# Kernel optimization log

Hardware: AMD Instinct MI355X
Metric: run time of the kernel (lower is better)

## Reference

```python
import jax, jax.numpy as jnp
import numpy as np

NEG_SLOPE = 0.2    # DenseGATConv attention leaky_relu slope (PyG default)
ACT_SLOPE = 0.01   # block activation LeakyReLU slope
HEADS = 3


def setup_inputs() -> dict:
    key = jax.random.key(0)
    B, N, D0, D1, D2, H = 512, 128, 128, 64, 64, HEADS
    ks = jax.random.split(key, 7)
    x = jax.random.normal(ks[0], (B * N, D0), jnp.float32)
    # equal-sized graphs: sorted graph ids, N atoms per graph
    batch_mask = jnp.repeat(jnp.arange(B, dtype=jnp.int32), N)
    s0 = 1.0 / np.sqrt(D0)
    s1 = 1.0 / np.sqrt(D1)
    s2 = 1.0 / np.sqrt(D2)
    W1 = jax.random.normal(ks[1], (D0, H * D1), jnp.float32) * s0
    att_src1 = jax.random.normal(ks[2], (H, D1), jnp.float32) * s1
    att_dst1 = jax.random.normal(ks[3], (H, D1), jnp.float32) * s1
    b1 = jnp.zeros((D1,), jnp.float32)
    W2 = jax.random.normal(ks[4], (D1, H * D2), jnp.float32) * s1
    att_src2 = jax.random.normal(ks[5], (H, D2), jnp.float32) * s2
    att_dst2 = jax.random.normal(ks[6], (H, D2), jnp.float32) * s2
    b2 = jnp.zeros((D2,), jnp.float32)
    return dict(x=x, batch_mask=batch_mask, W1=W1, att_src1=att_src1,
                att_dst1=att_dst1, b1=b1, W2=W2, att_src2=att_src2,
                att_dst2=att_dst2, b2=b2, batch_size=B, n_max=N)


def _dense_gat(x, adj, W, a_src, a_dst, b):
    # x: [B, N, Din], adj: [B, N, N] (self-loops already set). concat=False.
    B, N, _ = x.shape
    H, C = a_src.shape
    h = (x @ W).reshape(B, N, H, C)                       # lin (no bias)
    a_s = jnp.einsum('bnhc,hc->bnh', h, a_src)            # per-node src score
    a_d = jnp.einsum('bnhc,hc->bnh', h, a_dst)            # per-node dst score
    alpha = a_s[:, None, :, :] + a_d[:, :, None, :]       # [B, i, j, H]
    alpha = jax.nn.leaky_relu(alpha, NEG_SLOPE)
    alpha = jnp.where(adj[..., None] == 0, -jnp.inf, alpha)
    alpha = jax.nn.softmax(alpha, axis=2)                 # over source j
    out = jnp.einsum('bijh,bjhc->bihc', alpha, h)         # [B, N, H, C]
    return out.mean(axis=2) + b                           # concat=False -> head mean


def reference(x, batch_mask, W1, att_src1, att_dst1, b1,
              W2, att_src2, att_dst2, b2, batch_size, n_max):
    total, D0 = x.shape
    counts = jnp.bincount(batch_mask, length=batch_size)          # atoms per graph
    starts = jnp.cumsum(counts) - counts
    pos = jnp.arange(total) - starts[batch_mask]                  # slot within graph
    # to_dense_batch
    xd = jnp.zeros((batch_size, n_max, D0), x.dtype).at[batch_mask, pos].set(x)
    node_in = jnp.arange(n_max)[None, :] < counts[:, None]        # [B, N] valid mask
    # block adjacency: fully connected within each graph, diag zeroed...
    adj = (node_in[:, :, None] & node_in[:, None, :]).astype(x.dtype)
    # ...then DenseGATConv add_loop=True re-sets the full diagonal to 1
    adj = jnp.where(jnp.eye(n_max, dtype=bool), jnp.asarray(1.0, x.dtype), adj)
    h = _dense_gat(xd, adj, W1, att_src1, att_dst1, b1)
    h = jax.nn.leaky_relu(h, ACT_SLOPE)
    h = _dense_gat(h, adj, W2, att_src2, att_dst2, b2)
    h = jax.nn.leaky_relu(h, ACT_SLOPE)
    return jnp.sum(h, axis=1)                                     # sum pooling -> [B, D2]
```

## Files before the change

kernel.cpp:

```cpp
#include <hip/hip_runtime.h>
#include <stdint.h>

#define NROW 128

typedef __attribute__((ext_vector_type(8))) __bf16 bf16x8;
typedef __attribute__((ext_vector_type(4))) float  f32x4;

static __device__ __forceinline__ uint16_t f2bf(float f) {
    union { float f; uint32_t i; } v; v.f = f;
    uint32_t x = v.i;
    return (uint16_t)((x + 0x7FFFu + ((x >> 16) & 1u)) >> 16);
}
static __device__ __forceinline__ uint16_t bfbits(float f) {
    __bf16 h = (__bf16)f;
    union { __bf16 h; uint16_t u; } c; c.h = h; return c.u;
}
static __device__ __forceinline__ float fexp2(float x) {
#if __has_builtin(__builtin_amdgcn_exp2f)
    return __builtin_amdgcn_exp2f(x);
#else
    return exp2f(x);
#endif
}
static __device__ __forceinline__ float frcp(float x) {
#if __has_builtin(__builtin_amdgcn_rcpf)
    return __builtin_amdgcn_rcpf(x);
#else
    return 1.0f / x;
#endif
}

__global__ __launch_bounds__(256)
void prep_kernel(const float* __restrict__ W1, const float* __restrict__ as1,
                 const float* __restrict__ ad1,
                 const float* __restrict__ W2, const float* __restrict__ as2,
                 const float* __restrict__ ad2,
                 uint16_t* __restrict__ wT1x, uint16_t* __restrict__ wT2x)
{
    constexpr float LOG2E = 1.4426950408889634f;
    int bid = blockIdx.x, t = threadIdx.x;
    if (bid < 96) {
        int idx = bid * 256 + t;
        int c = idx >> 7, k = idx & 127;
        wT1x[c * 128 + k] = f2bf(W1[k * 192 + c]);
    } else if (bid < 144) {
        int idx = (bid - 96) * 256 + t;
        int c = idx >> 6, k = idx & 63;
        wT2x[c * 64 + k] = f2bf(W2[k * 192 + c]);
    } else if (bid == 144) {
#pragma unroll
        for (int e = 0; e < 3; ++e) {
            int idx = t + e * 256;
            if (idx < 768) {
                int j = idx >> 7, k = idx & 127, hd = j >> 1;
                const float* av = (j & 1) ? ad1 : as1;
                float s = 0.f;
                for (int c = 0; c < 64; ++c)
                    s += W1[k * 192 + hd * 64 + c] * av[hd * 64 + c];
                wT1x[(192 + j) * 128 + k] = f2bf(s * LOG2E);
            }
        }
#pragma unroll
        for (int e = 0; e < 5; ++e) {
            int idx = t + e * 256;
            if (idx < 1280) wT1x[198 * 128 + idx] = 0;
        }
    } else {
#pragma unroll
        for (int e = 0; e < 2; ++e) {
            int idx = t + e * 256;
            if (idx < 384) {
                int j = idx >> 6, k = idx & 63, hd = j >> 1;
                const float* av = (j & 1) ? ad2 : as2;
                float s = 0.f;
                for (int c = 0; c < 64; ++c)
                    s += W2[k * 192 + hd * 64 + c] * av[hd * 64 + c];
                wT2x[(192 + j) * 64 + k] = f2bf(s * LOG2E);
            }
        }
#pragma unroll
        for (int e = 0; e < 3; ++e) {
            int idx = t + e * 256;
            if (idx < 640) wT2x[198 * 64 + idx] = 0;
        }
    }
}

static __device__ __forceinline__ uint32_t hT_off(int row, int colbytes) {
    uint32_t bo = (uint32_t)(row * 256 + colbytes);
    return bo ^ (uint32_t)((row & 7) << 4);
}
#define S2 72

static __device__ __forceinline__
void scores_and_hT(const f32x4* hacc, uint16_t* hT, float* as_s, float* ad_s,
                   int i0, int lr, int lg)
{
    if (lr < 6) {
        float* dst = (lr & 1) ? ad_s : as_s;
        int hd = lr >> 1;
#pragma unroll
        for (int r = 0; r < 4; ++r)
            dst[hd * 128 + i0 + lg * 4 + r] = hacc[12][r];
    }
#pragma unroll
    for (int f = 0; f < 12; ++f) {
        uint32_t p0 = (uint32_t)bfbits(hacc[f][0]) | ((uint32_t)bfbits(hacc[f][1]) << 16);
        uint32_t p1 = (uint32_t)bfbits(hacc[f][2]) | ((uint32_t)bfbits(hacc[f][3]) << 16);
        *(uint2*)((char*)hT + hT_off(f * 16 + lr, (i0 + lg * 4) * 2)) = make_uint2(p0, p1);
    }
}

static __device__ __forceinline__
void softmax_pv(const uint16_t* hT, const float* as_s, const float* ad_s,
                f32x4* oacc, int i0, int lr, int lg)
{
#pragma unroll
    for (int f = 0; f < 4; ++f) oacc[f] = (f32x4){0.f, 0.f, 0.f, 0.f};

#pragma unroll
    for (int hd = 0; hd < 3; ++hd) {
        float ad  = ad_s[hd * 128 + i0 + lr];
        float adm = ad - 16.0f;
        float adn = 0.2f * ad - 16.0f;
        bf16x8 ap[4];
        float zp = 0.f;
#pragma unroll
        for (int q = 0; q < 4; ++q) {
            float4 s0 = *(const float4*)&as_s[hd * 128 + q * 32 + lg * 8];
            float4 s1 = *(const float4*)&as_s[hd * 128 + q * 32 + lg * 8 + 4];
            float sv[8] = {s0.x, s0.y, s0.z, s0.w, s1.x, s1.y, s1.z, s1.w};
#pragma unroll
            for (int m = 0; m < 8; ++m) {
                float ev = fexp2(fmaxf(sv[m] + adm, __builtin_fmaf(sv[m], 0.2f, adn)));
                zp += ev;
                ap[q][m] = (__bf16)ev;
            }
        }
        zp += __shfl_xor(zp, 16);
        zp += __shfl_xor(zp, 32);
        float inv = frcp(3.0f * zp);

        f32x4 tacc[4];
#pragma unroll
        for (int f = 0; f < 4; ++f) tacc[f] = (f32x4){0.f, 0.f, 0.f, 0.f};
#pragma unroll
        for (int q = 0; q < 4; ++q)
#pragma unroll
            for (int f = 0; f < 4; ++f) {
                bf16x8 bfv = *(const bf16x8*)((const char*)hT +
                                 hT_off(hd * 64 + f * 16 + lr, q * 64 + lg * 16));
                tacc[f] = __builtin_amdgcn_mfma_f32_16x16x32_bf16(ap[q], bfv, tacc[f], 0, 0, 0);
            }
        float invr[4];
#pragma unroll
        for (int r = 0; r < 4; ++r) invr[r] = __shfl(inv, lg * 4 + r);
#pragma unroll
        for (int f = 0; f < 4; ++f)
#pragma unroll
            for (int r = 0; r < 4; ++r) oacc[f][r] += tacc[f][r] * invr[r];
    }
}

__global__ __launch_bounds__(512, 4)
void fused_kernel(const float* __restrict__ x,
                  const uint16_t* __restrict__ wT1g, const uint16_t* __restrict__ wT2g,
                  const float* __restrict__ b1g, const float* __restrict__ b2g,
                  float* __restrict__ outp)
{
    __shared__ __align__(16) char smem[49152];
    __shared__ __align__(16) float as_s[3 * 128];
    __shared__ __align__(16) float ad_s[3 * 128];
    __shared__ float bia[128];
    __shared__ float pool_s[8 * 64];

    uint16_t* hT  = (uint16_t*)smem;
    uint16_t* x2T = (uint16_t*)smem;

    const int b = blockIdx.x, t = threadIdx.x;
    const int w = t >> 6, lr = t & 15, lg = (t >> 4) & 3;
    const int i0 = w * 16;

    bf16x8 afr[4];
    {
        const float* xg = x + ((long)b * NROW + i0 + lr) * 128;
        float4 r0[4], r1[4];
#pragma unroll
        for (int q = 0; q < 4; ++q) {
            r0[q] = *(const float4*)(xg + q * 32 + lg * 8);
            r1[q] = *(const float4*)(xg + q * 32 + lg * 8 + 4);
        }
#pragma unroll
        for (int q = 0; q < 4; ++q) {
            bf16x8 a;
            a[0] = (__bf16)r0[q].x; a[1] = (__bf16)r0[q].y;
            a[2] = (__bf16)r0[q].z; a[3] = (__bf16)r0[q].w;
            a[4] = (__bf16)r1[q].x; a[5] = (__bf16)r1[q].y;
            a[6] = (__bf16)r1[q].z; a[7] = (__bf16)r1[q].w;
            afr[q] = a;
        }
    }
    if (t < 64) bia[t] = b1g[t];
    else if (t < 128) bia[t] = b2g[t - 64];

    f32x4 hacc[13];
#pragma unroll
    for (int f = 0; f < 13; ++f) hacc[f] = (f32x4){0.f, 0.f, 0.f, 0.f};
    {
        const uint16_t* wb = wT1g + lr * 128 + lg * 8;
#pragma unroll
        for (int q = 0; q < 4; ++q)
#pragma unroll
            for (int f = 0; f < 13; ++f) {
                bf16x8 bfv = *(const bf16x8*)(wb + f * 2048 + q * 32);
                hacc[f] = __builtin_amdgcn_mfma_f32_16x16x32_bf16(afr[q], bfv, hacc[f], 0, 0, 0);
            }
    }

    scores_and_hT(hacc, hT, as_s, ad_s, i0, lr, lg);
    __syncthreads();

    f32x4 oacc[4];
    softmax_pv(hT, as_s, ad_s, oacc, i0, lr, lg);
    __syncthreads();

#pragma unroll
    for (int f = 0; f < 4; ++f) {
        int c = f * 16 + lr;
        float bv = bia[c];
#pragma unroll
        for (int r = 0; r < 4; ++r) {
            float v = oacc[f][r] + bv;
            v = fmaxf(v, 0.01f * v);
            x2T[(i0 + lg * 4 + r) * S2 + c] = bfbits(v);
        }
    }
    asm volatile("s_waitcnt lgkmcnt(0)" ::: "memory");
    __builtin_amdgcn_sched_barrier(0);

    bf16x8 af2[2];
#pragma unroll
    for (int q = 0; q < 2; ++q)
        af2[q] = *(const bf16x8*)&x2T[(i0 + lr) * S2 + q * 32 + lg * 8];
    __syncthreads();

#pragma unroll
    for (int f = 0; f < 13; ++f) hacc[f] = (f32x4){0.f, 0.f, 0.f, 0.f};
    {
        const uint16_t* wb = wT2g + lr * 64 + lg * 8;
#pragma unroll
        for (int q = 0; q < 2; ++q)
#pragma unroll
            for (int f = 0; f < 13; ++f) {
                bf16x8 bfv = *(const bf16x8*)(wb + f * 1024 + q * 32);
                hacc[f] = __builtin_amdgcn_mfma_f32_16x16x32_bf16(af2[q], bfv, hacc[f], 0, 0, 0);
            }
    }

    scores_and_hT(hacc, hT, as_s, ad_s, i0, lr, lg);
    __syncthreads();

    softmax_pv(hT, as_s, ad_s, oacc, i0, lr, lg);

#pragma unroll
    for (int f = 0; f < 4; ++f) {
        int c = f * 16 + lr;
        float bv = bia[64 + c];
        float s = 0.f;
#pragma unroll
        for (int r = 0; r < 4; ++r) {
            float v = oacc[f][r] + bv;
            v = fmaxf(v, 0.01f * v);
            s += v;
        }
        s += __shfl_xor(s, 16);
        s += __shfl_xor(s, 32);
        if (lg == 0) pool_s[w * 64 + c] = s;
    }
    __syncthreads();
    if (t < 64) {
        float s = 0.f;
#pragma unroll
        for (int q = 0; q < 8; ++q) s += pool_s[q * 64 + t];
        outp[(long)b * 64 + t] = s;
    }
}

extern "C" void kernel_launch(void* const* d_in, const int* in_sizes, int n_in,
                              void* d_out, int out_size, void* d_ws, size_t ws_size,
                              hipStream_t stream)
{
    const float* x   = (const float*)d_in[0];
    const float* W1  = (const float*)d_in[2];
    const float* as1 = (const float*)d_in[3];
    const float* ad1 = (const float*)d_in[4];
    const float* b1  = (const float*)d_in[5];
    const float* W2  = (const float*)d_in[6];
    const float* as2 = (const float*)d_in[7];
    const float* ad2 = (const float*)d_in[8];
    const float* b2  = (const float*)d_in[9];

    uint16_t* wT1x = (uint16_t*)d_ws;
    uint16_t* wT2x = wT1x + 208 * 128;

    prep_kernel<<<146, 256, 0, stream>>>(W1, as1, ad1, W2, as2, ad2, wT1x, wT2x);
    fused_kernel<<<512, 512, 0, stream>>>(x, wT1x, wT2x, b1, b2, (float*)d_out);
}
```

Baseline: 155.0 us.

## Stage GAT weights in LDS and split projection GEMM into 2x2 warp tiles

Layer 1 and layer 2 weight matrices are now cooperatively loaded into shared memory instead of each warp reading them from global memory. Each warp computes two 16-row tiles over half of the output column tiles (7 or 6 of 13), so every weight fragment is reused across two row tiles. The layer-2 weight load is prefetched into registers before the first softmax/PV phase to overlap with it. In exchange, LDS use grows, and extra barriers plus a register-staged prefetch are added, which may lower occupancy.

New measurement: 139.7 us. -9.9%, faster.

```diff
diff --git a/kernel.cpp b/kernel.cpp
--- a/kernel.cpp
+++ b/kernel.cpp
@@ -93,21 +93,33 @@
 #define S2 72
 
 static __device__ __forceinline__
-void scores_and_hT(const f32x4* hacc, uint16_t* hT, float* as_s, float* ad_s,
-                   int i0, int lr, int lg)
-{
-    if (lr < 6) {
+void scores_hT_2rt(const f32x4 hacc[2][7], uint16_t* hTp, float* as_s, float* ad_s,
+                   int wr, int wc, int lr, int lg)
+{
+    if (wc && lr < 6) {
         float* dst = (lr & 1) ? ad_s : as_s;
         int hd = lr >> 1;
 #pragma unroll
-        for (int r = 0; r < 4; ++r)
-            dst[hd * 128 + i0 + lg * 4 + r] = hacc[12][r];
-    }
-#pragma unroll
-    for (int f = 0; f < 12; ++f) {
-        uint32_t p0 = (uint32_t)bfbits(hacc[f][0]) | ((uint32_t)bfbits(hacc[f][1]) << 16);
-        uint32_t p1 = (uint32_t)bfbits(hacc[f][2]) | ((uint32_t)bfbits(hacc[f][3]) << 16);
-        *(uint2*)((char*)hT + hT_off(f * 16 + lr, (i0 + lg * 4) * 2)) = make_uint2(p0, p1);
+        for (int rt = 0; rt < 2; ++rt)
+#pragma unroll
+            for (int r = 0; r < 4; ++r)
+                dst[hd * 128 + wr * 32 + rt * 16 + lg * 4 + r] = hacc[rt][5][r];
+    }
+#pragma unroll
+    for (int fp = 0; fp < 7; ++fp) {
+        if (wc == 0 || fp < 5) {
+            int f = 7 * wc + fp;
+#pragma unroll
+            for (int rt = 0; rt < 2; ++rt) {
+                uint32_t p0 = (uint32_t)bfbits(hacc[rt][fp][0]) |
+                              ((uint32_t)bfbits(hacc[rt][fp][1]) << 16);
+                uint32_t p1 = (uint32_t)bfbits(hacc[rt][fp][2]) |
+                              ((uint32_t)bfbits(hacc[rt][fp][3]) << 16);
+                *(uint2*)((char*)hTp +
+                    hT_off(f * 16 + lr, (wr * 32 + rt * 16 + lg * 4) * 2)) =
+                    make_uint2(p0, p1);
+            }
+        }
     }
 }
 
@@ -168,22 +180,24 @@
                   const float* __restrict__ b1g, const float* __restrict__ b2g,
                   float* __restrict__ outp)
 {
-    __shared__ __align__(16) char smem[49152];
+    __shared__ __align__(16) char smem[53248];
     __shared__ __align__(16) float as_s[3 * 128];
     __shared__ __align__(16) float ad_s[3 * 128];
     __shared__ float bia[128];
     __shared__ float pool_s[8 * 64];
 
-    uint16_t* hT  = (uint16_t*)smem;
-    uint16_t* x2T = (uint16_t*)smem;
+    uint16_t* x2T  = (uint16_t*)smem;
+    uint16_t* wT2l = (uint16_t*)(smem + 128 * S2 * 2);
 
     const int b = blockIdx.x, t = threadIdx.x;
     const int w = t >> 6, lr = t & 15, lg = (t >> 4) & 3;
+    const int wr = w >> 1, wc = w & 1;
     const int i0 = w * 16;
 
-    bf16x8 afr[4];
-    {
-        const float* xg = x + ((long)b * NROW + i0 + lr) * 128;
+    bf16x8 afr[2][4];
+#pragma unroll
+    for (int rt = 0; rt < 2; ++rt) {
+        const float* xg = x + ((long)b * NROW + wr * 32 + rt * 16 + lr) * 128;
         float4 r0[4], r1[4];
 #pragma unroll
         for (int q = 0; q < 4; ++q) {
@@ -197,31 +211,55 @@
             a[2] = (__bf16)r0[q].z; a[3] = (__bf16)r0[q].w;
             a[4] = (__bf16)r1[q].x; a[5] = (__bf16)r1[q].y;
             a[6] = (__bf16)r1[q].z; a[7] = (__bf16)r1[q].w;
-            afr[q] = a;
+            afr[rt][q] = a;
+        }
+    }
+#pragma unroll
+    for (int p = 0; p < 7; ++p) {
+        int idx = t + p * 512;
+        if (idx < 3328) {
+            int row = idx >> 4, cb = (idx & 15) * 16;
+            *(uint4*)(smem + hT_off(row, cb)) = *(const uint4*)(wT1g + row * 128 + cb / 2);
         }
     }
     if (t < 64) bia[t] = b1g[t];
     else if (t < 128) bia[t] = b2g[t - 64];
-
-    f32x4 hacc[13];
-#pragma unroll
-    for (int f = 0; f < 13; ++f) hacc[f] = (f32x4){0.f, 0.f, 0.f, 0.f};
-    {
-        const uint16_t* wb = wT1g + lr * 128 + lg * 8;
-#pragma unroll
-        for (int q = 0; q < 4; ++q)
-#pragma unroll
-            for (int f = 0; f < 13; ++f) {
-                bf16x8 bfv = *(const bf16x8*)(wb + f * 2048 + q * 32);
-                hacc[f] = __builtin_amdgcn_mfma_f32_16x16x32_bf16(afr[q], bfv, hacc[f], 0, 0, 0);
-            }
-    }
-
-    scores_and_hT(hacc, hT, as_s, ad_s, i0, lr, lg);
-    __syncthreads();
+    __syncthreads();
+
+    f32x4 hacc[2][7];
+#pragma unroll
+    for (int rt = 0; rt < 2; ++rt)
+#pragma unroll
+        for (int f = 0; f < 7; ++f) hacc[rt][f] = (f32x4){0.f, 0.f, 0.f, 0.f};
+#pragma unroll
+    for (int q = 0; q < 4; ++q)
+#pragma unroll
+        for (int fp = 0; fp < 7; ++fp) {
+            if (wc == 0 || fp < 6) {
+                bf16x8 bfv = *(const bf16x8*)(smem +
+                                 hT_off((7 * wc + fp) * 16 + lr, q * 64 + lg * 16));
+                hacc[0][fp] = __builtin_amdgcn_mfma_f32_16x16x32_bf16(afr[0][q], bfv, hacc[0][fp], 0, 0, 0);
+                hacc[1][fp] = __builtin_amdgcn_mfma_f32_16x16x32_bf16(afr[1][q], bfv, hacc[1][fp], 0, 0, 0);
+            }
+        }
+    __syncthreads();
+
+    scores_hT_2rt(hacc, (uint16_t*)smem, as_s, ad_s, wr, wc, lr, lg);
+    __syncthreads();
+
+    uint4 wpre[4];
+#pragma unroll
+    for (int p = 0; p < 3; ++p) {
+        int idx = t + p * 512; int row = idx >> 3; int c8 = (idx & 7) * 8;
+        wpre[p] = *(const uint4*)(wT2g + row * 64 + c8);
+    }
+    if (t < 128) {
+        int idx = t + 1536; int row = idx >> 3; int c8 = (idx & 7) * 8;
+        wpre[3] = *(const uint4*)(wT2g + row * 64 + c8);
+    }
 
     f32x4 oacc[4];
-    softmax_pv(hT, as_s, ad_s, oacc, i0, lr, lg);
+    softmax_pv((const uint16_t*)smem, as_s, ad_s, oacc, i0, lr, lg);
     __syncthreads();
 
 #pragma unroll
@@ -235,32 +273,43 @@
             x2T[(i0 + lg * 4 + r) * S2 + c] = bfbits(v);
         }
     }
-    asm volatile("s_waitcnt lgkmcnt(0)" ::: "memory");
-    __builtin_amdgcn_sched_barrier(0);
-
-    bf16x8 af2[2];
+#pragma unroll
+    for (int p = 0; p < 3; ++p) {
+        int idx = t + p * 512; int row = idx >> 3; int c8 = (idx & 7) * 8;
+        *(uint4*)&wT2l[row * S2 + c8] = wpre[p];
+    }
+    if (t < 128) {
+        int idx = t + 1536; int row = idx >> 3; int c8 = (idx & 7) * 8;
+        *(uint4*)&wT2l[row * S2 + c8] = wpre[3];
+    }
+    __syncthreads();
+
+    bf16x8 af2[2][2];
+#pragma unroll
+    for (int rt = 0; rt < 2; ++rt)
+#pragma unroll
+        for (int q = 0; q < 2; ++q)
+            af2[rt][q] = *(const bf16x8*)&x2T[(wr * 32 + rt * 16 + lr) * S2 + q * 32 + lg * 8];
+#pragma unroll
+    for (int rt = 0; rt < 2; ++rt)
+#pragma unroll
+        for (int f = 0; f < 7; ++f) hacc[rt][f] = (f32x4){0.f, 0.f, 0.f, 0.f};
 #pragma unroll
     for (int q = 0; q < 2; ++q)
-        af2[q] = *(const bf16x8*)&x2T[(i0 + lr) * S2 + q * 32 + lg * 8];
-    __syncthreads();
-
-#pragma unroll
-    for (int f = 0; f < 13; ++f) hacc[f] = (f32x4){0.f, 0.f, 0.f, 0.f};
-    {
-        const uint16_t* wb = wT2g + lr * 64 + lg * 8;
-#pragma unroll
-        for (int q = 0; q < 2; ++q)
-#pragma unroll
-            for (int f = 0; f < 13; ++f) {
-                bf16x8 bfv = *(const bf16x8*)(wb + f * 1024 + q * 32);
-                hacc[f] = __builtin_amdgcn_mfma_f32_16x16x32_bf16(af2[q], bfv, hacc[f], 0, 0, 0);
-            }
-    }
-
-    scores_and_hT(hacc, hT, as_s, ad_s, i0, lr, lg);
-    __syncthreads();
-
-    softmax_pv(hT, as_s, ad_s, oacc, i0, lr, lg);
+#pragma unroll
+        for (int fp = 0; fp < 7; ++fp) {
+            if (wc == 0 || fp < 6) {
+                bf16x8 bfv = *(const bf16x8*)&wT2l[((7 * wc + fp) * 16 + lr) * S2 + q * 32 + lg * 8];
+                hacc[0][fp] = __builtin_amdgcn_mfma_f32_16x16x32_bf16(af2[0][q], bfv, hacc[0][fp], 0, 0, 0);
+                hacc[1][fp] = __builtin_amdgcn_mfma_f32_16x16x32_bf16(af2[1][q], bfv, hacc[1][fp], 0, 0, 0);
+            }
+        }
+    __syncthreads();
+
+    scores_hT_2rt(hacc, (uint16_t*)smem, as_s, ad_s, wr, wc, lr, lg);
+    __syncthreads();
+
+    softmax_pv((const uint16_t*)smem, as_s, ad_s, oacc, i0, lr, lg);
 
 #pragma unroll
     for (int f = 0; f < 4; ++f) {
```

## Stage GAT weights in LDS and interleave softmax exp with PV MFMAs

Applied to the files above, without the earlier changes.

Both layer weight matrices are now cooperatively copied into shared memory, with coalesced 16-byte loads, before the projection MFMAs. Each wave then reads its B fragments from LDS instead of issuing scattered per-lane global loads. The layer-2 weight prefetch is issued into registers before the layer-1 epilogue so its latency overlaps that work. The softmax loop now feeds each chunk of bf16 probabilities straight into the PV MFMAs instead of building all four chunks first, which cuts register pressure. The cost is a larger LDS allocation, which may lower occupancy, plus extra block barriers.

Measured after the change: 130.4 us. 1.19x faster.

```diff
diff --git a/kernel.cpp b/kernel.cpp
--- a/kernel.cpp
+++ b/kernel.cpp
@@ -123,35 +123,32 @@
         float ad  = ad_s[hd * 128 + i0 + lr];
         float adm = ad - 16.0f;
         float adn = 0.2f * ad - 16.0f;
-        bf16x8 ap[4];
         float zp = 0.f;
+        f32x4 tacc[4];
+#pragma unroll
+        for (int f = 0; f < 4; ++f) tacc[f] = (f32x4){0.f, 0.f, 0.f, 0.f};
 #pragma unroll
         for (int q = 0; q < 4; ++q) {
             float4 s0 = *(const float4*)&as_s[hd * 128 + q * 32 + lg * 8];
             float4 s1 = *(const float4*)&as_s[hd * 128 + q * 32 + lg * 8 + 4];
             float sv[8] = {s0.x, s0.y, s0.z, s0.w, s1.x, s1.y, s1.z, s1.w};
+            bf16x8 apq;
 #pragma unroll
             for (int m = 0; m < 8; ++m) {
                 float ev = fexp2(fmaxf(sv[m] + adm, __builtin_fmaf(sv[m], 0.2f, adn)));
                 zp += ev;
-                ap[q][m] = (__bf16)ev;
+                apq[m] = (__bf16)ev;
+            }
+#pragma unroll
+            for (int f = 0; f < 4; ++f) {
+                bf16x8 bfv = *(const bf16x8*)((const char*)hT +
+                                 hT_off(hd * 64 + f * 16 + lr, q * 64 + lg * 16));
+                tacc[f] = __builtin_amdgcn_mfma_f32_16x16x32_bf16(apq, bfv, tacc[f], 0, 0, 0);
             }
         }
         zp += __shfl_xor(zp, 16);
         zp += __shfl_xor(zp, 32);
         float inv = frcp(3.0f * zp);
-
-        f32x4 tacc[4];
-#pragma unroll
-        for (int f = 0; f < 4; ++f) tacc[f] = (f32x4){0.f, 0.f, 0.f, 0.f};
-#pragma unroll
-        for (int q = 0; q < 4; ++q)
-#pragma unroll
-            for (int f = 0; f < 4; ++f) {
-                bf16x8 bfv = *(const bf16x8*)((const char*)hT +
-                                 hT_off(hd * 64 + f * 16 + lr, q * 64 + lg * 16));
-                tacc[f] = __builtin_amdgcn_mfma_f32_16x16x32_bf16(ap[q], bfv, tacc[f], 0, 0, 0);
-            }
         float invr[4];
 #pragma unroll
         for (int r = 0; r < 4; ++r) invr[r] = __shfl(inv, lg * 4 + r);
@@ -168,14 +165,14 @@
                   const float* __restrict__ b1g, const float* __restrict__ b2g,
                   float* __restrict__ outp)
 {
-    __shared__ __align__(16) char smem[49152];
+    __shared__ __align__(16) char smem[53248];
     __shared__ __align__(16) float as_s[3 * 128];
     __shared__ __align__(16) float ad_s[3 * 128];
     __shared__ float bia[128];
     __shared__ float pool_s[8 * 64];
 
-    uint16_t* hT  = (uint16_t*)smem;
-    uint16_t* x2T = (uint16_t*)smem;
+    uint16_t* x2T  = (uint16_t*)smem;
+    uint16_t* wT2l = (uint16_t*)(smem + 128 * S2 * 2);
 
     const int b = blockIdx.x, t = threadIdx.x;
     const int w = t >> 6, lr = t & 15, lg = (t >> 4) & 3;
@@ -200,67 +197,90 @@
             afr[q] = a;
         }
     }
+#pragma unroll
+    for (int p = 0; p < 7; ++p) {
+        int idx = t + p * 512;
+        if (idx < 3328) {
+            int row = idx >> 4, cb = (idx & 15) * 16;
+            *(uint4*)(smem + hT_off(row, cb)) = *(const uint4*)(wT1g + row * 128 + cb / 2);
+        }
+    }
     if (t < 64) bia[t] = b1g[t];
     else if (t < 128) bia[t] = b2g[t - 64];
+    __syncthreads();
 
     f32x4 hacc[13];
 #pragma unroll
     for (int f = 0; f < 13; ++f) hacc[f] = (f32x4){0.f, 0.f, 0.f, 0.f};
+#pragma unroll
+    for (int q = 0; q < 4; ++q)
+#pragma unroll
+        for (int f = 0; f < 13; ++f) {
+            bf16x8 bfv = *(const bf16x8*)(smem + hT_off(f * 16 + lr, q * 64 + lg * 16));
+            hacc[f] = __builtin_amdgcn_mfma_f32_16x16x32_bf16(afr[q], bfv, hacc[f], 0, 0, 0);
+        }
+    __syncthreads();
+
+    scores_and_hT(hacc, (uint16_t*)smem, as_s, ad_s, i0, lr, lg);
+    __syncthreads();
+
+    f32x4 oacc[4];
+    softmax_pv((const uint16_t*)smem, as_s, ad_s, oacc, i0, lr, lg);
+    __syncthreads();
+
     {
-        const uint16_t* wb = wT1g + lr * 128 + lg * 8;
-#pragma unroll
-        for (int q = 0; q < 4; ++q)
-#pragma unroll
-            for (int f = 0; f < 13; ++f) {
-                bf16x8 bfv = *(const bf16x8*)(wb + f * 2048 + q * 32);
-                hacc[f] = __builtin_amdgcn_mfma_f32_16x16x32_bf16(afr[q], bfv, hacc[f], 0, 0, 0);
-            }
-    }
-
-    scores_and_hT(hacc, hT, as_s, ad_s, i0, lr, lg);
-    __syncthreads();
-
-    f32x4 oacc[4];
-    softmax_pv(hT, as_s, ad_s, oacc, i0, lr, lg);
-    __syncthreads();
-
-#pragma unroll
-    for (int f = 0; f < 4; ++f) {
-        int c = f * 16 + lr;
-        float bv = bia[c];
-#pragma unroll
-        for (int r = 0; r < 4; ++r) {
-            float v = oacc[f][r] + bv;
-            v = fmaxf(v, 0.01f * v);
-            x2T[(i0 + lg * 4 + r) * S2 + c] = bfbits(v);
-        }
-    }
-    asm volatile("s_waitcnt lgkmcnt(0)" ::: "memory");
-    __builtin_amdgcn_sched_barrier(0);
+        uint4 wpre[4];
+#pragma unroll
+        for (int p = 0; p < 3; ++p) {
+            int idx = t + p * 512; int row = idx >> 3; int c8 = (idx & 7) * 8;
+            wpre[p] = *(const uint4*)(wT2g + row * 64 + c8);
+        }
+        if (t < 128) {
+            int idx = t + 1536; int row = idx >> 3; int c8 = (idx & 7) * 8;
+            wpre[3] = *(const uint4*)(wT2g + row * 64 + c8);
+        }
+#pragma unroll
+        for (int f = 0; f < 4; ++f) {
+            int c = f * 16 + lr;
+            float bv = bia[c];
+#pragma unroll
+            for (int r = 0; r < 4; ++r) {
+                float v = oacc[f][r] + bv;
+                v = fmaxf(v, 0.01f * v);
+                x2T[(i0 + lg * 4 + r) * S2 + c] = bfbits(v);
+            }
+        }
+#pragma unroll
+        for (int p = 0; p < 3; ++p) {
+            int idx = t + p * 512; int row = idx >> 3; int c8 = (idx & 7) * 8;
+            *(uint4*)&wT2l[row * S2 + c8] = wpre[p];
+        }
+        if (t < 128) {
+            int idx = t + 1536; int row = idx >> 3; int c8 = (idx & 7) * 8;
+            *(uint4*)&wT2l[row * S2 + c8] = wpre[3];
+        }
+    }
+    __syncthreads();
 
     bf16x8 af2[2];
 #pragma unroll
     for (int q = 0; q < 2; ++q)
         af2[q] = *(const bf16x8*)&x2T[(i0 + lr) * S2 + q * 32 + lg * 8];
-    __syncthreads();
-
 #pragma unroll
     for (int f = 0; f < 13; ++f) hacc[f] = (f32x4){0.f, 0.f, 0.f, 0.f};
-    {
-        const uint16_t* wb = wT2g + lr * 64 + lg * 8;
-#pragma unroll
-        for (int q = 0; q < 2; ++q)
-#pragma unroll
-            for (int f = 0; f < 13; ++f) {
-                bf16x8 bfv = *(const bf16x8*)(wb + f * 1024 + q * 32);
-                hacc[f] = __builtin_amdgcn_mfma_f32_16x16x32_bf16(af2[q], bfv, hacc[f], 0, 0, 0);
-            }
-    }
-
-    scores_and_hT(hacc, hT, as_s, ad_s, i0, lr, lg);
-    __syncthreads();
-
-    softmax_pv(hT, as_s, ad_s, oacc, i0, lr, lg);
+#pragma unroll
+    for (int q = 0; q < 2; ++q)
+#pragma unroll
+        for (int f = 0; f < 13; ++f) {
+            bf16x8 bfv = *(const bf16x8*)&wT2l[(f * 16 + lr) * S2 + q * 32 + lg * 8];
+            hacc[f] = __builtin_amdgcn_mfma_f32_16x16x32_bf16(af2[q], bfv, hacc[f], 0, 0, 0);
+        }
+    __syncthreads();
+
+    scores_and_hT(hacc, (uint16_t*)smem, as_s, ad_s, i0, lr, lg);
+    __syncthreads();
+
+    softmax_pv((const uint16_t*)smem, as_s, ad_s, oacc, i0, lr, lg);
 
 #pragma unroll
     for (int f = 0; f < 4; ++f) {
```
